# Optimization experiments

Hardware: AMD Instinct MI355X
Metric: run time of the kernel (lower is better)

Reference implementation:

```python
import jax, jax.numpy as jnp
import numpy as np

EPS = 1e-8  # torch F.cosine_similarity eps

B, H, K = 64, 2048, 256


def setup_inputs() -> dict:
    key = jax.random.key(0)
    k1, k2, k3, k4 = jax.random.split(key, 4)
    input_state = jax.random.normal(k1, (B, H), dtype=jnp.float32)
    knowledge_base = jax.random.normal(k2, (K, B, H), dtype=jnp.float32)
    W = jax.random.normal(k3, (H, H), dtype=jnp.float32) / np.sqrt(H)
    b = jax.random.normal(k4, (H,), dtype=jnp.float32) * 0.02
    return {"input_state": input_state, "knowledge_base": knowledge_base, "W": W, "b": b}


def reference(input_state, knowledge_base, W, b):
    # linear projection (torch Linear: x @ W.T + b)
    q = input_state @ W.T + b                      # [B, H]
    kproj = jnp.einsum('kbh,oh->kbo', knowledge_base, W) + b  # [K, B, H]
    # cosine similarity over last dim, with torch-style eps clamp on norms
    qn = jnp.maximum(jnp.linalg.norm(q, axis=-1), EPS)        # [B]
    kn = jnp.maximum(jnp.linalg.norm(kproj, axis=-1), EPS)    # [K, B]
    dots = jnp.einsum('bh,kbh->kb', q, kproj)                 # [K, B]
    scores = dots / (qn[None, :] * kn)                        # [K, B]
    # softmax over the K knowledge items
    attn = jax.nn.softmax(scores, axis=0)                     # [K, B]
    # output = input + softmax-weighted sum of (raw) knowledge items
    out = input_state + jnp.einsum('kb,kbh->bh', attn, knowledge_base)
    return out
```

## Files before the change

kernel.cpp:

```cpp
#include <hip/hip_runtime.h>
#include <hip/hip_bf16.h>

typedef unsigned short u16;
typedef unsigned int u32;
typedef unsigned long long u64;
typedef __attribute__((ext_vector_type(8))) short short8;
typedef __attribute__((ext_vector_type(4))) float float4v;

#define B_DIM 64
#define H_DIM 2048
#define K_DIM 256
#define NTHR  256

#define WS_WBF   0ull
#define WS_AQ    (8388608ull)
#define WS_Q     (WS_AQ + 524288ull)
#define WS_KN2   (WS_Q + 524288ull)
#define WS_DOTS  (WS_KN2 + 65536ull)
#define WS_KBF   (WS_DOTS + 65536ull)

__device__ __forceinline__ u16 f2bf(float f) {
    unsigned int u = __float_as_uint(f);
    unsigned int r = (u + 0x7fffu + ((u >> 16) & 1u)) >> 16;
    return (u16)r;
}

__device__ __forceinline__ u64 pack4(float4v v) {
    u64 a0 = f2bf(v.x), a1 = f2bf(v.y), a2 = f2bf(v.z), a3 = f2bf(v.w);
    return a0 | (a1 << 16) | (a2 << 32) | (a3 << 48);
}

__device__ __forceinline__ void llds16(const u16* g, u16* l) {
    __builtin_amdgcn_global_load_lds(
        (__attribute__((address_space(1))) void*)g,
        (__attribute__((address_space(3))) void*)l, 16, 0, 0);
}

__device__ __forceinline__ void gemm0_tile(const u16* __restrict__ Aq, const u16* __restrict__ Wb,
                                           float* __restrict__ qout, u16* As, u16* Bs,
                                           int nt, int ksplit) {
    const int tid = threadIdx.x;
    const int wave = tid >> 6, lane = tid & 63;
    const int l15 = lane & 15, qd = lane >> 4;
    const int wm = wave >> 1, wn = wave & 1;
    const int n0 = nt * 128;
    const int grow = lane >> 2;
    const int gcol = (((lane & 3) ^ ((lane >> 3) & 3)) * 8);
    const int sw = (l15 >> 1) & 3;
    float4v acc[4][4] = {};
    const int kb0 = ksplit * 512;
    for (int kk = 0; kk < 16; ++kk) {
        const int k0 = kb0 + kk * 32;
        #pragma unroll
        for (int i = 0; i < 2; ++i) {
            const int r = wave * 32 + i * 16;
            llds16(Wb + (size_t)(n0 + r + grow) * H_DIM + k0 + gcol, &Bs[r * 32]);
            llds16(Aq + (size_t)(r + grow) * H_DIM + k0 + gcol, &As[r * 32]);
        }
        __syncthreads();
        short8 af[4], bf_[4];
        #pragma unroll
        for (int mi = 0; mi < 4; ++mi)
            af[mi] = *(const short8*)&As[(wm * 64 + mi * 16 + l15) * 32 + ((qd ^ sw) * 8)];
        #pragma unroll
        for (int ni = 0; ni < 4; ++ni)
            bf_[ni] = *(const short8*)&Bs[(wn * 64 + ni * 16 + l15) * 32 + ((qd ^ sw) * 8)];
        #pragma unroll
        for (int mi = 0; mi < 4; ++mi)
            #pragma unroll
            for (int ni = 0; ni < 4; ++ni)
                acc[mi][ni] = __builtin_amdgcn_mfma_f32_16x16x32_bf16(af[mi], bf_[ni], acc[mi][ni], 0, 0, 0);
        __syncthreads();
    }
    const int n0w = n0 + wn * 64;
    if (wm == 0) {
        #pragma unroll
        for (int mi = 0; mi < 4; ++mi)
            #pragma unroll
            for (int reg = 0; reg < 4; ++reg) {
                const int m = mi * 16 + qd * 4 + reg;
                #pragma unroll
                for (int ni = 0; ni < 4; ++ni)
                    atomicAdd(&qout[m * H_DIM + n0w + ni * 16 + l15], acc[mi][ni][reg]);
            }
    }
}

__device__ __forceinline__ void gemmC_tile(const u16* __restrict__ Kbf, const u16* __restrict__ Wb,
                                           const float* __restrict__ bias, const float* __restrict__ q,
                                           float* __restrict__ kn2, float* __restrict__ dots,
                                           u16* As, u16* Bs, int x) {
    const int tid = threadIdx.x;
    const int wave = tid >> 6, lane = tid & 63;
    const int l15 = lane & 15, qd = lane >> 4;
    const int wm = wave >> 1, wn = wave & 1;
    const int mt = (x >> 6) * 4 + (x & 3);
    const int nt = (x >> 2) & 15;
    const int m0 = mt * 128, n0 = nt * 128;
    const int grow = lane >> 2;
    const int gcol = (((lane & 3) ^ ((lane >> 3) & 3)) * 8);
    const int sw = (l15 >> 1) & 3;
    float4v acc[4][4] = {};
    for (int kk = 0; kk < 64; ++kk) {
        const int k0 = kk * 32;
        #pragma unroll
        for (int i = 0; i < 2; ++i) {
            const int r = wave * 32 + i * 16;
            llds16(Wb + (size_t)(n0 + r + grow) * H_DIM + k0 + gcol, &Bs[r * 32]);
            llds16(Kbf + (size_t)(m0 + r + grow) * H_DIM + k0 + gcol, &As[r * 32]);
        }
        __syncthreads();
        short8 af[4], bf_[4];
        #pragma unroll
        for (int mi = 0; mi < 4; ++mi)
            af[mi] = *(const short8*)&As[(wm * 64 + mi * 16 + l15) * 32 + ((qd ^ sw) * 8)];
        #pragma unroll
        for (int ni = 0; ni < 4; ++ni)
            bf_[ni] = *(const short8*)&Bs[(wn * 64 + ni * 16 + l15) * 32 + ((qd ^ sw) * 8)];
        #pragma unroll
        for (int mi = 0; mi < 4; ++mi)
            #pragma unroll
            for (int ni = 0; ni < 4; ++ni)
                acc[mi][ni] = __builtin_amdgcn_mfma_f32_16x16x32_bf16(af[mi], bf_[ni], acc[mi][ni], 0, 0, 0);
        __syncthreads();
    }
    const int n0w = n0 + wn * 64;
    float bv[4];
    #pragma unroll
    for (int ni = 0; ni < 4; ++ni) bv[ni] = bias[n0w + ni * 16 + l15];
    #pragma unroll
    for (int mi = 0; mi < 4; ++mi)
        #pragma unroll
        for (int reg = 0; reg < 4; ++reg) {
            const int mloc = mi * 16 + qd * 4 + reg;
            const int mg = m0 + wm * 64 + mloc;
            const float* qrow = q + mloc * H_DIM;
            float s2 = 0.f, sd = 0.f;
            #pragma unroll
            for (int ni = 0; ni < 4; ++ni) {
                const float y = acc[mi][ni][reg] + bv[ni];
                const float qv = qrow[n0w + ni * 16 + l15];
                s2 += y * y; sd += y * qv;
            }
            #pragma unroll
            for (int off = 1; off < 16; off <<= 1) {
                s2 += __shfl_xor(s2, off);
                sd += __shfl_xor(sd, off);
            }
            if (l15 == 0) {
                atomicAdd(&kn2[mg], s2);
                atomicAdd(&dots[mg], sd);
            }
        }
}

__global__ __launch_bounds__(256) void prep_kernel(
        const float* __restrict__ W, const float* __restrict__ input,
        const float* __restrict__ bias, u16* __restrict__ Wb,
        u16* __restrict__ Aq, float* __restrict__ q,
        float* __restrict__ kn2, float* __restrict__ dots) {
    const int gid = blockIdx.x * NTHR + threadIdx.x;
    ((u64*)Wb)[gid] = pack4(((const float4v*)W)[gid]);
    if (gid < 65536) {
        u64 v = 0;
        if (gid < 32768) v = pack4(((const float4v*)input)[gid]);
        ((u64*)Aq)[gid] = v;
    }
    if (gid < 32768)
        ((float4v*)q)[gid] = ((const float4v*)bias)[gid & 511];
    if (gid < 4096) ((float4v*)kn2)[gid] = float4v{0.f, 0.f, 0.f, 0.f};
    else if (gid < 8192) ((float4v*)dots)[gid - 4096] = float4v{0.f, 0.f, 0.f, 0.f};
}

__global__ __launch_bounds__(256, 4) void mid_kernel(
        const float* __restrict__ kb, const u16* __restrict__ Aq,
        const u16* __restrict__ Wb, float* __restrict__ q, u16* __restrict__ Kbf) {
    __shared__ __align__(16) u16 As[128 * 32];
    __shared__ __align__(16) u16 Bs[128 * 32];
    const int bid = blockIdx.x;
    if (bid < 64) {
        gemm0_tile(Aq, Wb, q, As, Bs, bid & 15, bid >> 4);
    } else {
        const float4v* s4 = (const float4v*)kb;
        u64* d8 = (u64*)Kbf;
        for (int i = (bid - 64) * NTHR + threadIdx.x; i < 8388608; i += 960 * NTHR)
            d8[i] = pack4(s4[i]);
    }
}

__global__ __launch_bounds__(256, 4) void gemm_kernel(
        const u16* __restrict__ Kbf, const u16* __restrict__ Wb,
        const float* __restrict__ bias, const float* __restrict__ q,
        float* __restrict__ kn2, float* __restrict__ dots) {
    __shared__ __align__(16) u16 As[128 * 32];
    __shared__ __align__(16) u16 Bs[128 * 32];
    gemmC_tile(Kbf, Wb, bias, q, kn2, dots, As, Bs, blockIdx.x);
}

__global__ __launch_bounds__(256) void final_kernel(
        const float* __restrict__ input, const u16* __restrict__ Kbf,
        const float* __restrict__ q, const float* __restrict__ kn2,
        const float* __restrict__ dots, float* __restrict__ out) {
    __shared__ float sm[K_DIM];
    __shared__ float buf[4];
    const int b = blockIdx.x >> 2, hc = blockIdx.x & 3, tid = threadIdx.x;
    float s = 0.f;
    #pragma unroll
    for (int i = 0; i < 8; ++i) {
        float v = q[b * H_DIM + i * 256 + tid];
        s += v * v;
    }
    #pragma unroll
    for (int o = 32; o >= 1; o >>= 1) s += __shfl_xor(s, o);
    if ((tid & 63) == 0) buf[tid >> 6] = s;
    __syncthreads();
    const float qn = fmaxf(sqrtf(buf[0] + buf[1] + buf[2] + buf[3]), 1e-8f);
    __syncthreads();
    const float kn = fmaxf(sqrtf(kn2[tid * B_DIM + b]), 1e-8f);
    const float sc = dots[tid * B_DIM + b] / (qn * kn);
    float mx = sc;
    #pragma unroll
    for (int o = 32; o >= 1; o >>= 1) mx = fmaxf(mx, __shfl_xor(mx, o));
    if ((tid & 63) == 0) buf[tid >> 6] = mx;
    __syncthreads();
    mx = fmaxf(fmaxf(buf[0], buf[1]), fmaxf(buf[2], buf[3]));
    __syncthreads();
    const float e = expf(sc - mx);
    float se = e;
    #pragma unroll
    for (int o = 32; o >= 1; o >>= 1) se += __shfl_xor(se, o);
    if ((tid & 63) == 0) buf[tid >> 6] = se;
    __syncthreads();
    se = buf[0] + buf[1] + buf[2] + buf[3];
    sm[tid] = e / se;
    __syncthreads();
    const u32* base = (const u32*)Kbf;
    const int h2 = hc * 256 + tid;
    float s0 = 0.f, s1 = 0.f;
    #pragma unroll 8
    for (int k = 0; k < K_DIM; ++k) {
        const u32 p = base[(size_t)(k * B_DIM + b) * (H_DIM / 2) + h2];
        const float a = sm[k];
        s0 += a * __uint_as_float(p << 16);
        s1 += a * __uint_as_float(p & 0xffff0000u);
    }
    const int h = h2 * 2;
    float2 iv = *(const float2*)&input[(size_t)b * H_DIM + h];
    float2 r; r.x = iv.x + s0; r.y = iv.y + s1;
    *(float2*)&out[(size_t)b * H_DIM + h] = r;
}

extern "C" void kernel_launch(void* const* d_in, const int* in_sizes, int n_in,
                              void* d_out, int out_size, void* d_ws, size_t ws_size,
                              hipStream_t stream) {
    const float* input = (const float*)d_in[0];
    const float* kb    = (const float*)d_in[1];
    const float* W     = (const float*)d_in[2];
    const float* bias  = (const float*)d_in[3];
    float* out = (float*)d_out;
    char* ws = (char*)d_ws;

    u16*   Wb   = (u16*)(ws + WS_WBF);
    u16*   Aq   = (u16*)(ws + WS_AQ);
    float* q    = (float*)(ws + WS_Q);
    float* kn2  = (float*)(ws + WS_KN2);
    float* dots = (float*)(ws + WS_DOTS);
    u16*   Kbf  = (u16*)(ws + WS_KBF);

    prep_kernel<<<4096, NTHR, 0, stream>>>(W, input, bias, Wb, Aq, q, kn2, dots);
    mid_kernel<<<1024, NTHR, 0, stream>>>(kb, Aq, Wb, q, Kbf);
    gemm_kernel<<<2048, NTHR, 0, stream>>>(Kbf, Wb, bias, q, kn2, dots);
    final_kernel<<<256, NTHR, 0, stream>>>(input, Kbf, q, kn2, dots, out);
}
```

Measured before the change: 395.8 us.

## Rewrite main GEMM as 256x256 tile with 4-stage async LDS pipeline

Replaces the 128x128-tile, 256-thread GEMM over the projected knowledge base with a 256x256 tile using 512 threads and a 4-deep ring of LDS buffers filled by direct global-to-LDS loads. Loads for step t+3 are issued while MFMAs run on step t, with explicit vmcnt waits, barriers and setprio around the MFMA bursts. The larger tiles halve global re-reads of the bf16 operands per FLOP and hide load latency that the old loop exposed. In exchange it needs 128KB dynamic LDS, more accumulator registers (8x4 float4 per thread), and correctness relies on hand-tuned waitcnt counts.

Measured after the change: 380.3 us. -3.9%, faster.

```diff
diff --git a/kernel.cpp b/kernel.cpp
--- a/kernel.cpp
+++ b/kernel.cpp
@@ -86,74 +86,6 @@
     }
 }
 
-__device__ __forceinline__ void gemmC_tile(const u16* __restrict__ Kbf, const u16* __restrict__ Wb,
-                                           const float* __restrict__ bias, const float* __restrict__ q,
-                                           float* __restrict__ kn2, float* __restrict__ dots,
-                                           u16* As, u16* Bs, int x) {
-    const int tid = threadIdx.x;
-    const int wave = tid >> 6, lane = tid & 63;
-    const int l15 = lane & 15, qd = lane >> 4;
-    const int wm = wave >> 1, wn = wave & 1;
-    const int mt = (x >> 6) * 4 + (x & 3);
-    const int nt = (x >> 2) & 15;
-    const int m0 = mt * 128, n0 = nt * 128;
-    const int grow = lane >> 2;
-    const int gcol = (((lane & 3) ^ ((lane >> 3) & 3)) * 8);
-    const int sw = (l15 >> 1) & 3;
-    float4v acc[4][4] = {};
-    for (int kk = 0; kk < 64; ++kk) {
-        const int k0 = kk * 32;
-        #pragma unroll
-        for (int i = 0; i < 2; ++i) {
-            const int r = wave * 32 + i * 16;
-            llds16(Wb + (size_t)(n0 + r + grow) * H_DIM + k0 + gcol, &Bs[r * 32]);
-            llds16(Kbf + (size_t)(m0 + r + grow) * H_DIM + k0 + gcol, &As[r * 32]);
-        }
-        __syncthreads();
-        short8 af[4], bf_[4];
-        #pragma unroll
-        for (int mi = 0; mi < 4; ++mi)
-            af[mi] = *(const short8*)&As[(wm * 64 + mi * 16 + l15) * 32 + ((qd ^ sw) * 8)];
-        #pragma unroll
-        for (int ni = 0; ni < 4; ++ni)
-            bf_[ni] = *(const short8*)&Bs[(wn * 64 + ni * 16 + l15) * 32 + ((qd ^ sw) * 8)];
-        #pragma unroll
-        for (int mi = 0; mi < 4; ++mi)
-            #pragma unroll
-            for (int ni = 0; ni < 4; ++ni)
-                acc[mi][ni] = __builtin_amdgcn_mfma_f32_16x16x32_bf16(af[mi], bf_[ni], acc[mi][ni], 0, 0, 0);
-        __syncthreads();
-    }
-    const int n0w = n0 + wn * 64;
-    float bv[4];
-    #pragma unroll
-    for (int ni = 0; ni < 4; ++ni) bv[ni] = bias[n0w + ni * 16 + l15];
-    #pragma unroll
-    for (int mi = 0; mi < 4; ++mi)
-        #pragma unroll
-        for (int reg = 0; reg < 4; ++reg) {
-            const int mloc = mi * 16 + qd * 4 + reg;
-            const int mg = m0 + wm * 64 + mloc;
-            const float* qrow = q + mloc * H_DIM;
-            float s2 = 0.f, sd = 0.f;
-            #pragma unroll
-            for (int ni = 0; ni < 4; ++ni) {
-                const float y = acc[mi][ni][reg] + bv[ni];
-                const float qv = qrow[n0w + ni * 16 + l15];
-                s2 += y * y; sd += y * qv;
-            }
-            #pragma unroll
-            for (int off = 1; off < 16; off <<= 1) {
-                s2 += __shfl_xor(s2, off);
-                sd += __shfl_xor(sd, off);
-            }
-            if (l15 == 0) {
-                atomicAdd(&kn2[mg], s2);
-                atomicAdd(&dots[mg], sd);
-            }
-        }
-}
-
 __global__ __launch_bounds__(256) void prep_kernel(
         const float* __restrict__ W, const float* __restrict__ input,
         const float* __restrict__ bias, u16* __restrict__ Wb,
@@ -188,13 +120,119 @@
     }
 }
 
-__global__ __launch_bounds__(256, 4) void gemm_kernel(
+__global__ __launch_bounds__(512, 2) void gemm_kernel(
         const u16* __restrict__ Kbf, const u16* __restrict__ Wb,
         const float* __restrict__ bias, const float* __restrict__ q,
         float* __restrict__ kn2, float* __restrict__ dots) {
-    __shared__ __align__(16) u16 As[128 * 32];
-    __shared__ __align__(16) u16 Bs[128 * 32];
-    gemmC_tile(Kbf, Wb, bias, q, kn2, dots, As, Bs, blockIdx.x);
+    extern __shared__ __align__(16) u16 lds[];
+    const int tid = threadIdx.x;
+    const int wave = tid >> 6, lane = tid & 63;
+    const int l15 = lane & 15, qd = lane >> 4;
+    const int wm = wave >> 2, wn = wave & 3;
+    const int nt = blockIdx.x & 7, mt = blockIdx.x >> 3;
+    const int m0 = mt * 256, n0 = nt * 256;
+    const int grow = wave * 16 + (lane >> 2);
+    const int gcol = (((lane & 3) ^ ((lane >> 3) & 3)) * 8);
+    const int sw = (l15 >> 1) & 3;
+
+    const u16* srcA = Kbf + (size_t)(m0 + grow) * H_DIM + gcol;
+    const u16* srcB = Wb + (size_t)(n0 + grow) * H_DIM + gcol;
+    u16* dstBase = lds + wave * 512;
+
+    auto stageA = [&](int t) {
+        u16* d = dstBase + (t & 3) * 16384;
+        const u16* s = srcA + t * 32;
+        llds16(s, d);
+        llds16(s + (size_t)128 * H_DIM, d + 4096);
+    };
+    auto stageB = [&](int t) {
+        u16* d = dstBase + (t & 3) * 16384 + 8192;
+        const u16* s = srcB + t * 32;
+        llds16(s, d);
+        llds16(s + (size_t)128 * H_DIM, d + 4096);
+    };
+
+    const int aoff = (wm * 128 + l15) * 32 + ((qd ^ sw) * 8);
+    const int boff = (wn * 64 + l15) * 32 + ((qd ^ sw) * 8);
+
+    float4v acc[8][4] = {};
+
+    stageA(0); stageB(0); stageA(1); stageB(1); stageA(2); stageB(2);
+    asm volatile("s_waitcnt vmcnt(8)" ::: "memory");
+    __builtin_amdgcn_sched_barrier(0);
+    __builtin_amdgcn_s_barrier();
+
+    for (int t = 0; t < 64; ++t) {
+        const u16* As = lds + (t & 3) * 16384;
+        const u16* Bs = As + 8192;
+        short8 af[4], bf_[4];
+        #pragma unroll
+        for (int ni = 0; ni < 4; ++ni)
+            bf_[ni] = *(const short8*)&Bs[boff + ni * 512];
+        #pragma unroll
+        for (int mi = 0; mi < 4; ++mi)
+            af[mi] = *(const short8*)&As[aoff + mi * 512];
+        if (t + 3 < 64) stageA(t + 3);
+        __builtin_amdgcn_s_barrier();
+        asm volatile("s_waitcnt lgkmcnt(0)" ::: "memory");
+        __builtin_amdgcn_sched_barrier(0);
+        __builtin_amdgcn_s_setprio(1);
+        #pragma unroll
+        for (int mi = 0; mi < 4; ++mi)
+            #pragma unroll
+            for (int ni = 0; ni < 4; ++ni)
+                acc[mi][ni] = __builtin_amdgcn_mfma_f32_16x16x32_bf16(af[mi], bf_[ni], acc[mi][ni], 0, 0, 0);
+        __builtin_amdgcn_s_setprio(0);
+        __builtin_amdgcn_s_barrier();
+        #pragma unroll
+        for (int mi = 0; mi < 4; ++mi)
+            af[mi] = *(const short8*)&As[aoff + (4 + mi) * 512];
+        if (t + 3 < 64) stageB(t + 3);
+        __builtin_amdgcn_s_barrier();
+        asm volatile("s_waitcnt lgkmcnt(0)" ::: "memory");
+        __builtin_amdgcn_sched_barrier(0);
+        __builtin_amdgcn_s_setprio(1);
+        #pragma unroll
+        for (int mi = 0; mi < 4; ++mi)
+            #pragma unroll
+            for (int ni = 0; ni < 4; ++ni)
+                acc[4 + mi][ni] = __builtin_amdgcn_mfma_f32_16x16x32_bf16(af[mi], bf_[ni], acc[4 + mi][ni], 0, 0, 0);
+        __builtin_amdgcn_s_setprio(0);
+        if (t <= 60)      { asm volatile("s_waitcnt vmcnt(8)" ::: "memory"); }
+        else if (t == 61) { asm volatile("s_waitcnt vmcnt(4)" ::: "memory"); }
+        else if (t == 62) { asm volatile("s_waitcnt vmcnt(0)" ::: "memory"); }
+        __builtin_amdgcn_sched_barrier(0);
+        __builtin_amdgcn_s_barrier();
+    }
+
+    const int n0w = n0 + wn * 64;
+    float bv[4];
+    #pragma unroll
+    for (int ni = 0; ni < 4; ++ni) bv[ni] = bias[n0w + ni * 16 + l15];
+    #pragma unroll
+    for (int mi = 0; mi < 8; ++mi)
+        #pragma unroll
+        for (int reg = 0; reg < 4; ++reg) {
+            const int mloc = mi * 16 + qd * 4 + reg;
+            const int mg = m0 + wm * 128 + mloc;
+            const float* qrow = q + (mloc & 63) * H_DIM;
+            float s2 = 0.f, sd = 0.f;
+            #pragma unroll
+            for (int ni = 0; ni < 4; ++ni) {
+                const float y = acc[mi][ni][reg] + bv[ni];
+                const float qv = qrow[n0w + ni * 16 + l15];
+                s2 += y * y; sd += y * qv;
+            }
+            #pragma unroll
+            for (int off = 1; off < 16; off <<= 1) {
+                s2 += __shfl_xor(s2, off);
+                sd += __shfl_xor(sd, off);
+            }
+            if (l15 == 0) {
+                atomicAdd(&kn2[mg], s2);
+                atomicAdd(&dots[mg], sd);
+            }
+        }
 }
 
 __global__ __launch_bounds__(256) void final_kernel(
@@ -267,8 +305,15 @@
     float* dots = (float*)(ws + WS_DOTS);
     u16*   Kbf  = (u16*)(ws + WS_KBF);
 
+    static int lds_set = 0;
+    if (!lds_set) {
+        hipFuncSetAttribute((const void*)gemm_kernel,
+                            hipFuncAttributeMaxDynamicSharedMemorySize, 131072);
+        lds_set = 1;
+    }
+
     prep_kernel<<<4096, NTHR, 0, stream>>>(W, input, bias, Wb, Aq, q, kn2, dots);
     mid_kernel<<<1024, NTHR, 0, stream>>>(kb, Aq, Wb, q, Kbf);
-    gemm_kernel<<<2048, NTHR, 0, stream>>>(Kbf, Wb, bias, q, kn2, dots);
+    gemm_kernel<<<512, 512, 131072, stream>>>(Kbf, Wb, bias, q, kn2, dots);
     final_kernel<<<256, NTHR, 0, stream>>>(input, Kbf, q, kn2, dots, out);
 }
```
